# Kernel tuning notes

Measured on AMD Instinct MI355X. Metric: run time of the kernel, lower is better.

## Reference

```python
import jax, jax.numpy as jnp
import numpy as np

B, S, N, D, T = 128, 128, 196, 512, 12


def setup_inputs() -> dict:
    key = jax.random.key(0)
    ks = jax.random.split(key, 20)
    nrm = lambda i, shape, s: jax.random.normal(ks[i], shape, jnp.float32) * s
    w = lambda i, shape: nrm(i, shape, 1.0 / np.sqrt(shape[-1]))
    return {
        "ctx": nrm(0, (B, S, D), 1.0),
        "q": nrm(1, (B, 2 * D), 1.0),
        "k": nrm(2, (B, D, N), 1.0),
        "mem0": nrm(3, (1, D), 0.02),
        "ctrl0": nrm(4, (1, D), 0.02),
        # ControlUnit params
        "Wp": w(5, (T, D, 2 * D)), "bp": jnp.zeros((T, D), jnp.float32),
        "Wcq": w(6, (D, 2 * D)), "bcq": jnp.zeros((D,), jnp.float32),
        "Wca": w(7, (1, D)), "bca": jnp.zeros((1,), jnp.float32),
        # ReadUnit params
        "Wrm": w(8, (D, D)), "brm": jnp.zeros((D,), jnp.float32),
        "Wrc": w(9, (D, 2 * D)), "brc": jnp.zeros((D,), jnp.float32),
        "Wra": w(10, (1, D)), "bra": jnp.zeros((1,), jnp.float32),
        # WriteUnit params
        "Wwc": w(11, (D, 2 * D)), "bwc": jnp.zeros((D,), jnp.float32),
    }


def reference(ctx, q, k, mem0, ctrl0, Wp, bp, Wcq, bcq, Wca, bca,
              Wrm, brm, Wrc, brc, Wra, bra, Wwc, bwc):
    b = q.shape[0]
    c = jnp.broadcast_to(ctrl0, (b, D))
    m = jnp.broadcast_to(mem0, (b, D))
    for t in range(T):
        # --- control unit (alpha_entmax with alpha=1.0 == softmax) ---
        p = q @ Wp[t].T + bp[t]                                # [B, D]
        cc = jnp.concatenate([c, p], axis=1) @ Wcq.T + bcq     # [B, D]
        ctx_p = cc[:, None, :] * ctx                           # [B, S, D]
        aw = jax.nn.softmax(ctx_p @ Wca.T + bca, axis=1)       # [B, S, 1]
        c = (aw * ctx).sum(axis=1)                             # [B, D]
        # --- read unit ---
        mm = (m @ Wrm.T + brm)[:, :, None]                     # [B, D, 1]
        kc = jnp.concatenate([mm * k, k], axis=1)              # [B, 2D, N]
        rc = kc.transpose(0, 2, 1) @ Wrc.T + brc               # [B, N, D]
        logit = ((rc * c[:, None, :]) @ Wra.T + bra)[..., 0]   # [B, N]
        rw = jax.nn.softmax(logit, axis=1)[:, None, :]         # [B, 1, N]
        r = (rw * k).sum(axis=2)                               # [B, D]
        # --- write unit (no self-attention / memory gate) ---
        m = jnp.concatenate([r, m], axis=1) @ Wwc.T + bwc      # [B, D]
    return m
```

## Files before the change

kernel.cpp:

```cpp
#include <hip/hip_runtime.h>
#include <hip/hip_bf16.h>
#include <cstdint>

#define D  512
#define D2 1024
#define BB 128
#define SS 128
#define NN 196
#define TT 12

typedef unsigned short u16;
typedef __attribute__((ext_vector_type(8))) short short8v;
typedef __attribute__((ext_vector_type(4))) float f32x4;

__device__ __forceinline__ float bf2f(u16 h){
  union { unsigned int u; float f; } v; v.u = ((unsigned int)h) << 16; return v.f;
}

__device__ __forceinline__ float LDX(const void* p, size_t i, int isbf){
  if (isbf) return bf2f(((const u16*)p)[i]);
  return ((const float*)p)[i];
}

__device__ __forceinline__ float4 LD4(const void* p, size_t i, int isbf){
  if (isbf){
    ushort4 w = *(const ushort4*)((const u16*)p + i);
    return make_float4(bf2f(w.x), bf2f(w.y), bf2f(w.z), bf2f(w.w));
  }
  return *(const float4*)((const float*)p + i);
}

__device__ __forceinline__ void bfsplit(float x, short &h, short &l){
  unsigned u = __float_as_uint(x);
  unsigned hu = u & 0xFFFF0000u;
  float r = x - __uint_as_float(hu);
  h = (short)(u >> 16);
  l = (short)(__float_as_uint(r) >> 16);
}

__global__ __launch_bounds__(256) void k_detect(const u16* ctx, int* flag){
  __shared__ int cnt;
  if (threadIdx.x == 0) cnt = 0;
  __syncthreads();
  int bad = 0;
  for (int i = threadIdx.x; i < 8192; i += 256){
    int e = (ctx[i] >> 7) & 0xFF;
    if (e == 0xFF || (e != 0 && (e < 90 || e > 160))) bad++;
  }
  atomicAdd(&cnt, bad);
  __syncthreads();
  if (threadIdx.x == 0) *flag = (cnt > 100) ? 0 : 1;
}

__global__ __launch_bounds__(256) void k_prep1(const void* Wcq, const void* Wca,
      const void* Wwc, const void* Wrm, const void* Wrc, const void* Wra,
      const void* bp, const void* bcq, const void* ctrl0, const void* mem0, const void* brm,
      float* W1f, float* Wwcf, float* WrmTf, float* W2f,
      float* P, float* pp2, float* ubase, float* mmb, const int* flag){
  const int isbf = *flag;
  __shared__ float lds[32][33];
  int bk = blockIdx.x, tid = threadIdx.x;
  int tx = tid & 31, ty = tid >> 5;
  if (bk >= 1216){
    int ib = bk - 1216;
    int lane = tid & 63, w = tid >> 6;
    int grp = lane >> 3, k = lane & 7;
    int isU = (ib < 16);
    int o = (isU ? ib : ib - 16)*32 + w*8 + grp;
    const void* vec = isU ? ctrl0 : mem0;
    const void* mat = isU ? Wcq : Wrm;
    int ld = isU ? D2 : D;
    float acc = 0.f;
    #pragma unroll 4
    for (int it = 0; it < 16; it++){
      int d = it*32 + k*4;
      float4 v = LD4(vec, d, isbf);
      float4 m = LD4(mat, (size_t)o*ld + d, isbf);
      acc += v.x*m.x + v.y*m.y + v.z*m.z + v.w*m.w;
    }
    acc += __shfl_xor(acc, 1, 64);
    acc += __shfl_xor(acc, 2, 64);
    acc += __shfl_xor(acc, 4, 64);
    if (k == 0){
      if (isU) ubase[o] = acc * LDX(Wca, o, isbf);
      else     mmb[o]   = acc + LDX(brm, o, isbf);
    }
    return;
  }
  if (bk >= 1152){
    int l = bk - 1152;
    for (int idx = l*256 + tid; idx < 786432; idx += 64*256){
      int j = (idx >> 7) & 511;
      pp2[idx] = LDX(bcq, j, isbf) * LDX(Wca, j, isbf);
    }
    return;
  }
  if (bk >= 1088){
    int l = bk - 1088;
    for (int idx = l*256 + tid; idx < 786432; idx += 64*256)
      P[idx] = LDX(bp, idx >> 7, isbf);
    return;
  }
  if (bk >= 1024){
    int l = bk - 1024;
    if (isbf){
      const u16* w = (const u16*)Wrc; const u16* s = (const u16*)Wra;
      for (int idx = l*256 + tid; idx < 524288; idx += 64*256)
        W2f[idx] = bf2f(w[idx]) * bf2f(s[idx >> 10]);
    } else {
      const float* w = (const float*)Wrc; const float* s = (const float*)Wra;
      for (int idx = l*256 + tid; idx < 524288; idx += 64*256)
        W2f[idx] = w[idx] * s[idx >> 10];
    }
    return;
  }
  const void* in = nullptr; const void* scale = nullptr; float* out = nullptr;
  int ld = 0, R = 0, tR = 0, tC = 0;
  if (bk < 256)      { int l = bk;       in = Wcq; ld = 1024; R = 512; out = W1f;  scale = Wca; tR = l & 15; tC = l >> 4; }
  else if (bk < 768) { int l = bk - 256; in = Wwc; ld = 1024; R = 512; out = Wwcf; tR = l & 15; tC = l >> 4; }
  else               { int l = bk - 768; in = Wrm; ld = 512;  R = 512; out = WrmTf;tR = l & 15; tC = l >> 4; }
  int r0 = tR*32, c0 = tC*32;
  #pragma unroll
  for (int kk = 0; kk < 4; kk++){
    int r = r0 + ty + kk*8;
    float v = LDX(in, (size_t)r*ld + c0 + tx, isbf);
    if (scale) v *= LDX(scale, r, isbf);
    lds[tx][ty + kk*8] = v;
  }
  __syncthreads();
  #pragma unroll
  for (int kk = 0; kk < 4; kk++){
    int oc = ty + kk*8;
    out[(size_t)(c0 + oc)*R + r0 + tx] = lds[oc][tx];
  }
}

__global__ __launch_bounds__(256) void k_pack(const void* q, u16* QF,
                                              const void* kmat, float* kT, const int* flag){
  const int isbf = *flag;
  __shared__ float lds[64][201];
  int bk = blockIdx.x, tid = threadIdx.x;
  if (bk < 128){
    u16* QH = QF;
    u16* QL = QF + 131072;
    for (int idx = bk*256 + tid; idx < 131072; idx += 128*256){
      int b = idx >> 10, x = idx & 1023;
      int o = ((x >> 3) << 10) + (b << 3) + (x & 7);
      if (isbf){
        QH[o] = ((const u16*)q)[idx];
        QL[o] = 0;
      } else {
        short h, l;
        bfsplit(((const float*)q)[idx], h, l);
        QH[o] = (u16)h;
        QL[o] = (u16)l;
      }
    }
    return;
  }
  int l = bk - 128;
  int b = l >> 3, dt = l & 7;
  int d0 = dt*64;
  int r = tid >> 2, q4 = tid & 3;
  const size_t rowbase = ((size_t)b*D + d0 + r)*NN;
  #pragma unroll
  for (int p = 0; p < 13; p++){
// ... 88 lines not shown
    const u16* w = (const u16*)Wcq;
    for (int e = e0k; e < e0k + 256; e += 8){
      float a[8];
      #pragma unroll
      for (int u = 0; u < 8; u++) a[u] = P[(size_t)(t*D + e + u)*BB + b];
      #pragma unroll
      for (int kk = 0; kk < 4; kk++){
        ushort4 w0 = *(const ushort4*)(w + (size_t)(j0+kk)*D2 + D + e);
        ushort4 w1 = *(const ushort4*)(w + (size_t)(j0+kk)*D2 + D + e + 4);
        acc[kk] += a[0]*bf2f(w0.x) + a[1]*bf2f(w0.y) + a[2]*bf2f(w0.z) + a[3]*bf2f(w0.w)
                 + a[4]*bf2f(w1.x) + a[5]*bf2f(w1.y) + a[6]*bf2f(w1.z) + a[7]*bf2f(w1.w);
      }
    }
  } else {
    const float* w = (const float*)Wcq;
    for (int e = e0k; e < e0k + 256; e += 8){
      float a[8];
      #pragma unroll
      for (int u = 0; u < 8; u++) a[u] = P[(size_t)(t*D + e + u)*BB + b];
      #pragma unroll
      for (int kk = 0; kk < 4; kk++){
        float4 w0 = *(const float4*)(w + (size_t)(j0+kk)*D2 + D + e);
        float4 w1 = *(const float4*)(w + (size_t)(j0+kk)*D2 + D + e + 4);
        acc[kk] += a[0]*w0.x + a[1]*w0.y + a[2]*w0.z + a[3]*w0.w
                 + a[4]*w1.x + a[5]*w1.y + a[6]*w1.z + a[7]*w1.w;
      }
    }
  }
  #pragma unroll
  for (int kk = 0; kk < 4; kk++)
    atomicAdd(&pp2[(size_t)(t*D + j0 + kk)*BB + b], acc[kk] * LDX(Wca, j0 + kk, isbf));
}

__global__ __launch_bounds__(256) void k_initB(const float* ubase, const float* mmb,
                                               const void* mem0, const float* pp2,
                                               float* u0, float* mm0, float* act0,
                                               const int* flag){
  const int isbf = *flag;
  for (int idx = blockIdx.x*256 + threadIdx.x; idx < 3*D*BB; idx += 96*256){
    if (idx < D*BB)            u0[idx] = ubase[idx >> 7] + pp2[idx];
    else if (idx < 2*D*BB)   { int x = idx - D*BB;   mm0[x] = mmb[x >> 7]; }
    else                     { int x = idx - 2*D*BB; act0[D*BB + x] = LDX(mem0, x >> 7, isbf); }
  }
}

__global__ __launch_bounds__(512) void k_K1(const void* ctx, const float* u_cur,
                                            float* gbuf, const float* pbuf, const float* kT,
                                            float* r_out, int t, const int* flag){
  __shared__ float sm[1024];
  int bk = blockIdx.x, tid = threadIdx.x;
  const int isbf = *flag;
  if (bk < 512){
    if (t == 0) return;
    float* lg   = sm;
    float* red  = sm + 256;
    float* psum = sm + 512;
    int b = bk & 127, qc = bk >> 7;
    if (tid < 256){
      float s;
      if (tid < NN){
        s = 0.f;
        #pragma unroll
        for (int c = 0; c < 8; c++)
          s += pbuf[((size_t)c*BB + b)*256 + tid];
      } else s = -INFINITY;
      lg[tid] = s; red[tid] = s;
    }
    __syncthreads();
    for (int off = 128; off; off >>= 1){ if (tid < off) red[tid] = fmaxf(red[tid], red[tid+off]); __syncthreads(); }
    float M = red[0];
    __syncthreads();
    if (tid < 256){ float e = (tid < NN) ? __expf(lg[tid] - M) : 0.f; lg[tid] = e; red[tid] = e; }
    __syncthreads();
    for (int off = 128; off; off >>= 1){ if (tid < off) red[tid] += red[tid+off]; __syncthreads(); }
    float inv = 1.f / red[0];
    int ng = tid >> 7, dl = tid & 127;
    const float* kTb = kT + ((size_t)b*NN + ng*49)*D + qc*128 + dl;
    float acc = 0.f;
    for (int j = 0; j < 49; j++)
      acc += lg[ng*49 + j] * kTb[(size_t)j*D];
    psum[ng*128 + dl] = acc;
    __syncthreads();
    if (tid < 128)
      r_out[(size_t)(qc*128 + tid)*BB + b] =
        (psum[tid] + psum[128 + tid] + psum[256 + tid] + psum[384 + tid]) * inv;
    return;
  }
  if (t >= TT) return;
  int l = bk - 512;
  int b = l & 127, sc = l >> 7;
  float* us = sm;
  us[tid] = u_cur[(size_t)tid*BB + b];
  __syncthreads();
  int lane = tid & 63, wv = tid >> 6;
  float ur[8];
  #pragma unroll
  for (int j = 0; j < 8; j++) ur[j] = us[lane*8 + j];
  #pragma unroll
  for (int rr = 0; rr < 4; rr++){
    int s = sc*32 + wv*4 + rr;
    size_t base = ((size_t)(b*SS + s))*D + lane*8;
    float4 c0 = LD4(ctx, base, isbf);
    float4 c1 = LD4(ctx, base + 4, isbf);
    float dot = ur[0]*c0.x + ur[1]*c0.y + ur[2]*c0.z + ur[3]*c0.w
              + ur[4]*c1.x + ur[5]*c1.y + ur[6]*c1.z + ur[7]*c1.w;
    #pragma unroll
    for (int off = 32; off; off >>= 1) dot += __shfl_down(dot, off, 64);
    if (lane == 0) gbuf[b*SS + s] = dot;
  }
}

__global__ __launch_bounds__(512) void k_K2(const void* ctx, const float* gbuf, float* cbuf,
                                            const float* act_prev, float* act_cur,
                                            float* wbuf, float* mmbuf, float* u_nxt,
                                            const float* pp2_next, const void* brm,
                                            const float* Wwcf, int t, const int* flag){
  __shared__ float sm[768];
  int bk = blockIdx.x, tid = threadIdx.x;
  const int isbf = *flag;
  if (bk < 512){
    float* lg   = sm;
    float* red  = sm + 128;
    float* psum = sm + 256;
    int b = bk & 127, qc = bk >> 7;
    if (tid < 128){ float v = gbuf[b*SS + tid]; lg[tid] = v; red[tid] = v; }
    __syncthreads();
    for (int off = 64; off; off >>= 1){ if (tid < off) red[tid] = fmaxf(red[tid], red[tid+off]); __syncthreads(); }
    float M = red[0];
    __syncthreads();
    if (tid < 128){ float e = __expf(lg[tid] - M); lg[tid] = e; red[tid] = e; }
    __syncthreads();
    for (int off = 64; off; off >>= 1){ if (tid < off) red[tid] += red[tid+off]; __syncthreads(); }
    float inv = 1.f / red[0];
    int sg = tid >> 7, dl = tid & 127;
    int d = qc*128 + dl;
    float acc = 0.f;
    for (int j = 0; j < 32; j++){
      int s = sg*32 + j;
      acc += lg[s] * LDX(ctx, ((size_t)(b*SS + s))*D + d, isbf);
    }
    psum[sg*128 + dl] = acc;
    __syncthreads();
    if (tid < 128)
      cbuf[(size_t)(qc*128 + tid)*BB + b] =
        (psum[tid] + psum[128 + tid] + psum[256 + tid] + psum[384 + tid]) * inv;
    return;
  }
  int b = tid & 127;
  int ih = __builtin_amdgcn_readfirstlane(tid >> 7);
  if (bk < 1024){
    if (t == 0) return;
    int l = bk - 512;
    int it = l >> 3, kc = l & 7;
    int ih0 = ih & 1, ih1 = ih >> 1;
    int i0 = it*8 + ih0*4;
    int e0 = kc*128 + ih1*64;
    float acc[4] = {0.f,0.f,0.f,0.f};
    for (int e = e0; e < e0 + 64; e += 8){
      float av[8];
      #pragma unroll
      for (int u = 0; u < 8; u++) av[u] = act_prev[(size_t)(e+u)*BB + b];
      #pragma unroll
      for (int u = 0; u < 8; u++){
        float4 w0 = *(const float4*)(Wwcf + (size_t)(e+u)*D + i0);
        acc[0]+=av[u]*w0.x; acc[1]+=av[u]*w0.y; acc[2]+=av[u]*w0.z; acc[3]+=av[u]*w0.w;
      }
    }
    #pragma unroll
    for (int kk = 0; kk < 4; kk++)
      atomicAdd(&act_cur[(size_t)(D + i0 + kk)*BB + b], acc[kk]);
  } else if (bk < 1088){
    int l = bk - 1024;
    for (int x = l*512 + tid; x < D2*BB; x += 64*512) wbuf[x] = 0.f;
  } else if (bk < 1120){
    if (t == 0) return;
    int l = bk - 1088;
    for (int x = l*512 + tid; x < D*BB; x += 32*512) mmbuf[x] = LDX(brm, x >> 7, isbf);
  } else {
    if (t >= TT-1) return;
    int l = bk - 1120;
    for (int x = l*512 + tid; x < D*BB; x += 32*512) u_nxt[x] = pp2_next[x];
  }
}

__global__ __launch_bounds__(256) void k_KB(const float* cbuf, const float* W2f, float* wbuf,
                                            const float* act_cur, const float* WrmTf,
                                            float* mmbuf, int t){
  int bk = blockIdx.x, tid = threadIdx.x;
  int b = tid & 127;
  int ih = __builtin_amdgcn_readfirstlane(tid >> 7);
  if (bk < 512){
    int et = bk >> 2, kc = bk & 3;
    int e0 = et*8 + ih*4;
    float acc[4] = {0.f, 0.f, 0.f, 0.f};
    int j0 = kc*128;
    for (int j = j0; j < j0 + 128; j += 8){
      float av[8];
      #pragma unroll
      for (int u = 0; u < 8; u++) av[u] = cbuf[(j+u)*BB + b];
      #pragma unroll
      for (int u = 0; u < 8; u++){
        float4 wv = *(const float4*)(W2f + (size_t)(j+u)*D2 + e0);
        acc[0] += av[u]*wv.x; acc[1] += av[u]*wv.y;
        acc[2] += av[u]*wv.z; acc[3] += av[u]*wv.w;
      }
    }
    #pragma unroll
    for (int kk = 0; kk < 4; kk++) atomicAdd(&wbuf[(e0+kk)*BB + b], acc[kk]);
  } else {
    if (t == 0) return;
    int l = bk - 512;
    int it = l >> 2, kc = l & 3;
    int i0 = it*8 + ih*4;
    float acc[4] = {0.f, 0.f, 0.f, 0.f};
    int d0 = kc*128;
    for (int d = d0; d < d0 + 128; d += 8){
      float av[8];
      #pragma unroll
      for (int u = 0; u < 8; u++) av[u] = act_cur[(size_t)(D + d + u)*BB + b];
      #pragma unroll
      for (int u = 0; u < 8; u++){
        float4 wv = *(const float4*)(WrmTf + (size_t)(d+u)*D + i0);
        acc[0] += av[u]*wv.x; acc[1] += av[u]*wv.y;
        acc[2] += av[u]*wv.z; acc[3] += av[u]*wv.w;
      }
    }
    #pragma unroll
    for (int kk = 0; kk < 4; kk++) atomicAdd(&mmbuf[(i0+kk)*BB + b], acc[kk]);
  }
}

__global__ __launch_bounds__(512) void k_KC1(const void* kmat, const float* wbuf,
                                             const float* mmbuf, float* pbuf,
                                             const float* cbuf, const float* W1f, float* u_nxt,
                                             float* act_nxt, const void* bwc,
                                             int t, const int* flag){
  __shared__ float u2[128];
  int bk = blockIdx.x, tid = threadIdx.x;
  const int isbf = *flag;
  if (bk < 512){
    int b = bk & 127, ch2 = bk >> 7;
    int d0 = ch2*128;
    if (tid < 128){
      int d = d0 + tid;
      u2[tid] = wbuf[(size_t)d*BB + b]*mmbuf[(size_t)d*BB + b] + wbuf[(size_t)(D + d)*BB + b];
    }
    __syncthreads();
    int half = tid >> 8;
    int n = tid & 255;
    int dd0 = half*64;
    float part = 0.f;
    if (n < NN){
      float c[8];
      #pragma unroll
      for (int u = 0; u < 8; u++) c[u] = 0.f;
      if (isbf){
        const u16* kb = (const u16*)kmat + (size_t)b*D*NN + (size_t)(d0+dd0)*NN + n;
        for (int dd = 0; dd < 64; dd += 8){
          #pragma unroll
          for (int u = 0; u < 8; u++) c[u] += u2[dd0+dd+u]*bf2f(kb[(size_t)(dd+u)*NN]);
        }
      } else {
        const float* kb = (const float*)kmat + (size_t)b*D*NN + (size_t)(d0+dd0)*NN + n;
        for (int dd = 0; dd < 64; dd += 8){
          #pragma unroll
          for (int u = 0; u < 8; u++) c[u] += u2[dd0+dd+u]*kb[(size_t)(dd+u)*NN];
        }
      }
      part = (((c[0]+c[1]) + (c[2]+c[3])) + ((c[4]+c[5]) + (c[6]+c[7])));
    }
    int chunk = ch2*2 + half;
    pbuf[((size_t)chunk*BB + b)*256 + n] = part;
    return;
  }
  int b = tid & 127;
  int ih = __builtin_amdgcn_readfirstlane(tid >> 7);
  if (bk < 768){
    if (t >= TT-1) return;
    int l = bk - 512;
// ... 73 lines not shown
    }
  }
}

extern "C" void kernel_launch(void* const* d_in, const int* in_sizes, int n_in,
                              void* d_out, int out_size, void* d_ws, size_t ws_size,
                              hipStream_t stream){
  const void* ctx  = d_in[0];
  const void* q    = d_in[1];
  const void* kmat = d_in[2];
  const void* mem0 = d_in[3];
  const void* ctrl0= d_in[4];
  const void* Wp   = d_in[5];
  const void* bp   = d_in[6];
  const void* Wcq  = d_in[7];
  const void* bcq  = d_in[8];
  const void* Wca  = d_in[9];
  const void* Wrm  = d_in[11];
  const void* brm  = d_in[12];
  const void* Wrc  = d_in[13];
  const void* Wra  = d_in[15];
  const void* Wwc  = d_in[17];
  const void* bwc  = d_in[18];

  float* W      = (float*)d_ws;
  float* qT     = W;
  float* P      = W + 131072;
  float* pp2    = W + 917504;
  float* W1f    = W + 1703936;
  float* W2f    = W + 1966080;
  float* Wwcf   = W + 2490368;
  float* WrmTf  = W + 3014656;
  float* cbuf   = W + 3276800;
  float* wbuf   = W + 3342336;
  float* mmbuf  = W + 3473408;
  float* actb   = W + 3538944;
  float* ubuf   = W + 3801088;
  int*   flag   = (int*)(W + 3932160);
  float* ubase  = W + 3932224;
  float* mmb    = W + 3932736;
  float* gbuf   = W + 3933248;
  float* pbuf   = P;
  float* kT     = W + 4194304;

  hipLaunchKernelGGL(k_detect, dim3(1), dim3(256), 0, stream, (const u16*)ctx, flag);
  hipLaunchKernelGGL(k_prep1, dim3(1248), dim3(256), 0, stream,
                     Wcq, Wca, Wwc, Wrm, Wrc, Wra, bp, bcq, ctrl0, mem0, brm,
                     W1f, Wwcf, WrmTf, W2f, P, pp2, ubase, mmb, flag);
  hipLaunchKernelGGL(k_pack, dim3(1152), dim3(256), 0, stream,
                     q, (u16*)qT, kmat, kT, flag);
  hipLaunchKernelGGL(k_Pmfma, dim3(768), dim3(256), 0, stream, Wp, (const u16*)qT, P, flag);
  hipLaunchKernelGGL(k_pp2,  dim3(768), dim3(512), 0, stream, P, Wcq, Wca, pp2, flag);
  hipLaunchKernelGGL(k_initB, dim3(96), dim3(256), 0, stream,
                     ubase, mmb, mem0, pp2, ubuf, mmbuf, actb, flag);

  for (int t = 0; t < TT; t++){
    int cur = t & 1, nxt = 1 - cur;
    float* act_cur  = actb + cur*131072;
    float* act_prev = actb + nxt*131072;
    hipLaunchKernelGGL(k_K1, dim3(1024), dim3(512), 0, stream,
                       ctx, ubuf + cur*65536, gbuf, pbuf, kT,
                       act_prev, t, flag);
    hipLaunchKernelGGL(k_K2, dim3(1152), dim3(512), 0, stream,
                       ctx, gbuf, cbuf, act_prev, act_cur,
                       wbuf, mmbuf, ubuf + nxt*65536,
                       pp2 + ((t+1 < TT) ? (t+1)*65536 : 0), brm, Wwcf, t, flag);
    hipLaunchKernelGGL(k_KB, dim3(768), dim3(256), 0, stream,
                       cbuf, W2f, wbuf, act_cur, WrmTf, mmbuf, t);
    hipLaunchKernelGGL(k_KC1, dim3(800), dim3(512), 0, stream,
                       kmat, wbuf, mmbuf, pbuf,
                       cbuf, W1f, ubuf + nxt*65536,
                       actb + nxt*131072, bwc, t, flag);
  }
  hipLaunchKernelGGL(k_K1, dim3(512), dim3(512), 0, stream,
                     ctx, ubuf, gbuf, pbuf, kT,
                     actb + 131072, TT, flag);
  hipLaunchKernelGGL(k_moutA, dim3(512), dim3(512), 0, stream,
                     actb + 131072, Wwcf, actb);
  hipLaunchKernelGGL(k_outT, dim3(64), dim3(256), 0, stream, actb, d_out, flag);
}
```

Before: 1.017 ms.

## Precompose Wwc·Wrm and merge attention kernels to cut per-step launches

```diff
diff --git a/kernel.cpp b/kernel.cpp
--- a/kernel.cpp
+++ b/kernel.cpp
@@ -55,8 +55,9 @@
 __global__ __launch_bounds__(256) void k_prep1(const void* Wcq, const void* Wca,
       const void* Wwc, const void* Wrm, const void* Wrc, const void* Wra,
       const void* bp, const void* bcq, const void* ctrl0, const void* mem0, const void* brm,
+      const void* bwc,
       float* W1f, float* Wwcf, float* WrmTf, float* W2f,
-      float* P, float* pp2, float* ubase, float* mmb, const int* flag){
+      float* P, float* pp2, float* ubase, float* mmb, float* mmc, const int* flag){
   const int isbf = *flag;
   __shared__ float lds[32][33];
   int bk = blockIdx.x, tid = threadIdx.x;
@@ -65,11 +66,11 @@
     int ib = bk - 1216;
     int lane = tid & 63, w = tid >> 6;
     int grp = lane >> 3, k = lane & 7;
-    int isU = (ib < 16);
-    int o = (isU ? ib : ib - 16)*32 + w*8 + grp;
-    const void* vec = isU ? ctrl0 : mem0;
-    const void* mat = isU ? Wcq : Wrm;
-    int ld = isU ? D2 : D;
+    int kind = ib >> 4;
+    int o = (ib & 15)*32 + w*8 + grp;
+    const void* vec = (kind == 0) ? ctrl0 : ((kind == 1) ? mem0 : bwc);
+    const void* mat = (kind == 0) ? Wcq : Wrm;
+    int ld = (kind == 0) ? D2 : D;
     float acc = 0.f;
     #pragma unroll 4
     for (int it = 0; it < 16; it++){
@@ -82,8 +83,9 @@
     acc += __shfl_xor(acc, 2, 64);
     acc += __shfl_xor(acc, 4, 64);
     if (k == 0){
-      if (isU) ubase[o] = acc * LDX(Wca, o, isbf);
-      else     mmb[o]   = acc + LDX(brm, o, isbf);
+      if (kind == 0)      ubase[o] = acc * LDX(Wca, o, isbf);
+      else if (kind == 1) mmb[o]   = acc + LDX(brm, o, isbf);
+      else                mmc[o]   = acc + LDX(brm, o, isbf);
     }
     return;
   }
@@ -132,6 +134,26 @@
   for (int kk = 0; kk < 4; kk++){
     int oc = ty + kk*8;
     out[(size_t)(c0 + oc)*R + r0 + tx] = lds[oc][tx];
+  }
+}
+
+__global__ __launch_bounds__(256) void k_gf(const float* Wwcf, const float* WrmTf, float* GF){
+  __shared__ float wr[4][512];
+  int o0 = blockIdx.x * 4, tid = threadIdx.x;
+  for (int idx = tid; idx < 4*512; idx += 256)
+    wr[idx >> 9][idx & 511] = Wwcf[(size_t)(o0 + (idx >> 9))*D + (idx & 511)];
+  __syncthreads();
+  float a0[4] = {0.f,0.f,0.f,0.f}, a1[4] = {0.f,0.f,0.f,0.f};
+  for (int j = 0; j < 512; j++){
+    float x = WrmTf[(size_t)j*D + tid];
+    float y = WrmTf[(size_t)j*D + 256 + tid];
+    #pragma unroll
+    for (int r = 0; r < 4; r++){ a0[r] += wr[r][j]*x; a1[r] += wr[r][j]*y; }
+  }
+  #pragma unroll
+  for (int r = 0; r < 4; r++){
+    GF[(size_t)(o0 + r)*D + tid]       = a0[r];
+    GF[(size_t)(o0 + r)*D + 256 + tid] = a1[r];
   }
 }
 
@@ -298,9 +320,10 @@
   }
 }
 
-__global__ __launch_bounds__(512) void k_K1(const void* ctx, const float* u_cur,
-                                            float* gbuf, const float* pbuf, const float* kT,
-                                            float* r_out, int t, const int* flag){
+__global__ __launch_bounds__(512) void k_KA2(const void* ctx, const float* u_cur,
+      const float* pbuf, const float* kT, float* cbuf, float* r_out,
+      float* wbuf, float* mmbuf, float* u_nxt, const float* pp2_next,
+      const float* mmb, const float* mmc, int t, const int* flag){
   __shared__ float sm[1024];
   int bk = blockIdx.x, tid = threadIdx.x;
   const int isbf = *flag;
@@ -340,44 +363,31 @@
         (psum[tid] + psum[128 + tid] + psum[256 + tid] + psum[384 + tid]) * inv;
     return;
   }
-  if (t >= TT) return;
-  int l = bk - 512;
-  int b = l & 127, sc = l >> 7;
-  float* us = sm;
-  us[tid] = u_cur[(size_t)tid*BB + b];
-  __syncthreads();
-  int lane = tid & 63, wv = tid >> 6;
-  float ur[8];
-  #pragma unroll
-  for (int j = 0; j < 8; j++) ur[j] = us[lane*8 + j];
-  #pragma unroll
-  for (int rr = 0; rr < 4; rr++){
-    int s = sc*32 + wv*4 + rr;
-    size_t base = ((size_t)(b*SS + s))*D + lane*8;
-    float4 c0 = LD4(ctx, base, isbf);
-    float4 c1 = LD4(ctx, base + 4, isbf);
-    float dot = ur[0]*c0.x + ur[1]*c0.y + ur[2]*c0.z + ur[3]*c0.w
-              + ur[4]*c1.x + ur[5]*c1.y + ur[6]*c1.z + ur[7]*c1.w;
-    #pragma unroll
-    for (int off = 32; off; off >>= 1) dot += __shfl_down(dot, off, 64);
-    if (lane == 0) gbuf[b*SS + s] = dot;
-  }
-}
-
-__global__ __launch_bounds__(512) void k_K2(const void* ctx, const float* gbuf, float* cbuf,
-                                            const float* act_prev, float* act_cur,
-                                            float* wbuf, float* mmbuf, float* u_nxt,
-                                            const float* pp2_next, const void* brm,
-                                            const float* Wwcf, int t, const int* flag){
-  __shared__ float sm[768];
-  int bk = blockIdx.x, tid = threadIdx.x;
-  const int isbf = *flag;
-  if (bk < 512){
-    float* lg   = sm;
-    float* red  = sm + 128;
-    float* psum = sm + 256;
-    int b = bk & 127, qc = bk >> 7;
-    if (tid < 128){ float v = gbuf[b*SS + tid]; lg[tid] = v; red[tid] = v; }
+  if (bk < 640){
+    if (t >= TT) return;
+    int b = bk - 512;
+    float* us  = sm;
+    float* lg  = sm + 512;
+    float* red = sm + 640;
+    us[tid] = u_cur[(size_t)tid*BB + b];
+    __syncthreads();
+    int lane = tid & 63, wv = tid >> 6;
+    float ur[8];
+    #pragma unroll
+    for (int j = 0; j < 8; j++) ur[j] = us[lane*8 + j];
+    for (int rr = 0; rr < 16; rr++){
+      int s = wv*16 + rr;
+      size_t base = ((size_t)(b*SS + s))*D + lane*8;
+      float4 c0 = LD4(ctx, base, isbf);
+      float4 c1 = LD4(ctx, base + 4, isbf);
+      float dot = ur[0]*c0.x + ur[1]*c0.y + ur[2]*c0.z + ur[3]*c0.w
+                + ur[4]*c1.x + ur[5]*c1.y + ur[6]*c1.z + ur[7]*c1.w;
+      #pragma unroll
+      for (int off = 32; off; off >>= 1) dot += __shfl_down(dot, off, 64);
+      if (lane == 0) lg[s] = dot;
+    }
+    __syncthreads();
+    if (tid < 128) red[tid] = lg[tid];
     __syncthreads();
     for (int off = 64; off; off >>= 1){ if (tid < off) red[tid] = fmaxf(red[tid], red[tid+off]); __syncthreads(); }
     float M = red[0];
@@ -386,66 +396,37 @@
     __syncthreads();
     for (int off = 64; off; off >>= 1){ if (tid < off) red[tid] += red[tid+off]; __syncthreads(); }
     float inv = 1.f / red[0];
-    int sg = tid >> 7, dl = tid & 127;
-    int d = qc*128 + dl;
     float acc = 0.f;
-    for (int j = 0; j < 32; j++){
-      int s = sg*32 + j;
-      acc += lg[s] * LDX(ctx, ((size_t)(b*SS + s))*D + d, isbf);
-    }
-    psum[sg*128 + dl] = acc;
-    __syncthreads();
-    if (tid < 128)
-      cbuf[(size_t)(qc*128 + tid)*BB + b] =
-        (psum[tid] + psum[128 + tid] + psum[256 + tid] + psum[384 + tid]) * inv;
-    return;
-  }
-  int b = tid & 127;
-  int ih = __builtin_amdgcn_readfirstlane(tid >> 7);
-  if (bk < 1024){
-    if (t == 0) return;
-    int l = bk - 512;
-    int it = l >> 3, kc = l & 7;
-    int ih0 = ih & 1, ih1 = ih >> 1;
-    int i0 = it*8 + ih0*4;
-    int e0 = kc*128 + ih1*64;
-    float acc[4] = {0.f,0.f,0.f,0.f};
-    for (int e = e0; e < e0 + 64; e += 8){
-      float av[8];
-      #pragma unroll
-      for (int u = 0; u < 8; u++) av[u] = act_prev[(size_t)(e+u)*BB + b];
-      #pragma unroll
-      for (int u = 0; u < 8; u++){
-        float4 w0 = *(const float4*)(Wwcf + (size_t)(e+u)*D + i0);
-        acc[0]+=av[u]*w0.x; acc[1]+=av[u]*w0.y; acc[2]+=av[u]*w0.z; acc[3]+=av[u]*w0.w;
-      }
-    }
-    #pragma unroll
-    for (int kk = 0; kk < 4; kk++)
-      atomicAdd(&act_cur[(size_t)(D + i0 + kk)*BB + b], acc[kk]);
-  } else if (bk < 1088){
-    int l = bk - 1024;
-    for (int x = l*512 + tid; x < D2*BB; x += 64*512) wbuf[x] = 0.f;
-  } else if (bk < 1120){
-    if (t == 0) return;
-    int l = bk - 1088;
-    for (int x = l*512 + tid; x < D*BB; x += 32*512) mmbuf[x] = LDX(brm, x >> 7, isbf);
+    #pragma unroll 8
+    for (int s = 0; s < SS; s++)
+      acc += lg[s] * LDX(ctx, ((size_t)(b*SS + s))*D + tid, isbf);
+    cbuf[(size_t)tid*BB + b] = acc * inv;
+    return;
+  }
+  if (bk < 656){
+    int l = bk - 640;
+    for (int x = l*512 + tid; x < D2*BB; x += 16*512) wbuf[x] = 0.f;
+  } else if (bk < 664){
+    int l = bk - 656;
+    const float* src = (t == 0) ? mmb : mmc;
+    for (int x = l*512 + tid; x < D*BB; x += 8*512) mmbuf[x] = src[x >> 7];
   } else {
     if (t >= TT-1) return;
-    int l = bk - 1120;
-    for (int x = l*512 + tid; x < D*BB; x += 32*512) u_nxt[x] = pp2_next[x];
-  }
-}
-
-__global__ __launch_bounds__(256) void k_KB(const float* cbuf, const float* W2f, float* wbuf,
-                                            const float* act_cur, const float* WrmTf,
-                                            float* mmbuf, int t){
+    int l = bk - 664;
+    for (int x = l*512 + tid; x < D*BB; x += 8*512) u_nxt[x] = pp2_next[x];
+  }
+}
+
+__global__ __launch_bounds__(512) void k_KB2(const float* cbuf, const float* W2f, float* wbuf,
+                                             const float* act_prev, const float* GF,
+                                             float* mmbuf, const float* Wwcf, float* act_cur,
+                                             int t){
   int bk = blockIdx.x, tid = threadIdx.x;
   int b = tid & 127;
   int ih = __builtin_amdgcn_readfirstlane(tid >> 7);
-  if (bk < 512){
+  if (bk < 256){
     int et = bk >> 2, kc = bk & 3;
-    int e0 = et*8 + ih*4;
+    int e0 = et*16 + ih*4;
     float acc[4] = {0.f, 0.f, 0.f, 0.f};
     int j0 = kc*128;
     for (int j = j0; j < j0 + 128; j += 8){
@@ -461,27 +442,31 @@
     }
     #pragma unroll
     for (int kk = 0; kk < 4; kk++) atomicAdd(&wbuf[(e0+kk)*BB + b], acc[kk]);
-  } else {
-    if (t == 0) return;
-    int l = bk - 512;
-    int it = l >> 2, kc = l & 3;
-    int i0 = it*8 + ih*4;
-    float acc[4] = {0.f, 0.f, 0.f, 0.f};
-    int d0 = kc*128;
-    for (int d = d0; d < d0 + 128; d += 8){
-      float av[8];
-      #pragma unroll
-      for (int u = 0; u < 8; u++) av[u] = act_cur[(size_t)(D + d + u)*BB + b];
-      #pragma unroll
-      for (int u = 0; u < 8; u++){
-        float4 wv = *(const float4*)(WrmTf + (size_t)(d+u)*D + i0);
-        acc[0] += av[u]*wv.x; acc[1] += av[u]*wv.y;
-        acc[2] += av[u]*wv.z; acc[3] += av[u]*wv.w;
-      }
-    }
-    #pragma unroll
-    for (int kk = 0; kk < 4; kk++) atomicAdd(&mmbuf[(i0+kk)*BB + b], acc[kk]);
-  }
+    return;
+  }
+  if (t == 0) return;
+  const float* Mx; float* outp; int obase;
+  int l;
+  if (bk < 768){ l = bk - 256; Mx = GF;   outp = mmbuf;   obase = 0; }
+  else         { l = bk - 768; Mx = Wwcf; outp = act_cur; obase = D; }
+  int it = l >> 3, kc = l & 7;
+  int ih0 = ih & 1, ih1 = ih >> 1;
+  int i0 = it*8 + ih0*4;
+  int e0 = kc*128 + ih1*64;
+  float acc[4] = {0.f,0.f,0.f,0.f};
+  for (int e = e0; e < e0 + 64; e += 8){
+    float av[8];
+    #pragma unroll
+    for (int u = 0; u < 8; u++) av[u] = act_prev[(size_t)(e+u)*BB + b];
+    #pragma unroll
+    for (int u = 0; u < 8; u++){
+      float4 w0 = *(const float4*)(Mx + (size_t)(e+u)*D + i0);
+      acc[0]+=av[u]*w0.x; acc[1]+=av[u]*w0.y; acc[2]+=av[u]*w0.z; acc[3]+=av[u]*w0.w;
+    }
+  }
+  #pragma unroll
+  for (int kk = 0; kk < 4; kk++)
+    atomicAdd(&outp[(size_t)(obase + i0 + kk)*BB + b], acc[kk]);
 }
 
 __global__ __launch_bounds__(512) void k_KC1(const void* kmat, const float* wbuf,
@@ -645,17 +630,19 @@
   int*   flag   = (int*)(W + 3932160);
   float* ubase  = W + 3932224;
   float* mmb    = W + 3932736;
-  float* gbuf   = W + 3933248;
+  float* mmc    = W + 3933248;
   float* pbuf   = P;
   float* kT     = W + 4194304;
+  float* GF     = W + 17039360;
 
   hipLaunchKernelGGL(k_detect, dim3(1), dim3(256), 0, stream, (const u16*)ctx, flag);
-  hipLaunchKernelGGL(k_prep1, dim3(1248), dim3(256), 0, stream,
-                     Wcq, Wca, Wwc, Wrm, Wrc, Wra, bp, bcq, ctrl0, mem0, brm,
-                     W1f, Wwcf, WrmTf, W2f, P, pp2, ubase, mmb, flag);
+  hipLaunchKernelGGL(k_prep1, dim3(1264), dim3(256), 0, stream,
+                     Wcq, Wca, Wwc, Wrm, Wrc, Wra, bp, bcq, ctrl0, mem0, brm, bwc,
+                     W1f, Wwcf, WrmTf, W2f, P, pp2, ubase, mmb, mmc, flag);
   hipLaunchKernelGGL(k_pack, dim3(1152), dim3(256), 0, stream,
                      q, (u16*)qT, kmat, kT, flag);
   hipLaunchKernelGGL(k_Pmfma, dim3(768), dim3(256), 0, stream, Wp, (const u16*)qT, P, flag);
+  hipLaunchKernelGGL(k_gf, dim3(256), dim3(256), 0, stream, Wwcf, WrmTf, GF);
   hipLaunchKernelGGL(k_pp2,  dim3(768), dim3(512), 0, stream, P, Wcq, Wca, pp2, flag);
   hipLaunchKernelGGL(k_initB, dim3(96), dim3(256), 0, stream,
                      ubase, mmb, mem0, pp2, ubuf, mmbuf, actb, flag);
@@ -664,23 +651,20 @@
     int cur = t & 1, nxt = 1 - cur;
     float* act_cur  = actb + cur*131072;
     float* act_prev = actb + nxt*131072;
-    hipLaunchKernelGGL(k_K1, dim3(1024), dim3(512), 0, stream,
-                       ctx, ubuf + cur*65536, gbuf, pbuf, kT,
-                       act_prev, t, flag);
-    hipLaunchKernelGGL(k_K2, dim3(1152), dim3(512), 0, stream,
-                       ctx, gbuf, cbuf, act_prev, act_cur,
+    hipLaunchKernelGGL(k_KA2, dim3(672), dim3(512), 0, stream,
+                       ctx, ubuf + cur*65536, pbuf, kT, cbuf, act_prev,
                        wbuf, mmbuf, ubuf + nxt*65536,
-                       pp2 + ((t+1 < TT) ? (t+1)*65536 : 0), brm, Wwcf, t, flag);
-    hipLaunchKernelGGL(k_KB, dim3(768), dim3(256), 0, stream,
-                       cbuf, W2f, wbuf, act_cur, WrmTf, mmbuf, t);
+                       pp2 + ((t+1 < TT) ? (t+1)*65536 : 0), mmb, mmc, t, flag);
+    hipLaunchKernelGGL(k_KB2, dim3(1280), dim3(512), 0, stream,
+                       cbuf, W2f, wbuf, act_prev, GF, mmbuf, Wwcf, act_cur, t);
     hipLaunchKernelGGL(k_KC1, dim3(800), dim3(512), 0, stream,
                        kmat, wbuf, mmbuf, pbuf,
                        cbuf, W1f, ubuf + nxt*65536,
                        actb + nxt*131072, bwc, t, flag);
   }
-  hipLaunchKernelGGL(k_K1, dim3(512), dim3(512), 0, stream,
-                     ctx, ubuf, gbuf, pbuf, kT,
-                     actb + 131072, TT, flag);
+  hipLaunchKernelGGL(k_KA2, dim3(512), dim3(512), 0, stream,
+                     ctx, ubuf, pbuf, kT, cbuf, actb + 131072,
+                     wbuf, mmbuf, ubuf, pp2, mmb, mmc, TT, flag);
   hipLaunchKernelGGL(k_moutA, dim3(512), dim3(512), 0, stream,
                      actb + 131072, Wwcf, actb);
   hipLaunchKernelGGL(k_outT, dim3(64), dim3(256), 0, stream, actb, d_out, flag);
```

Result: slower. 1.102 ms (+8.4%).

## Precompose Wrm with Wwc to compute next-step mm directly from previous activations

Applied to the files above, without the earlier changes.

```diff
diff --git a/kernel.cpp b/kernel.cpp
--- a/kernel.cpp
+++ b/kernel.cpp
@@ -55,8 +55,9 @@
 __global__ __launch_bounds__(256) void k_prep1(const void* Wcq, const void* Wca,
       const void* Wwc, const void* Wrm, const void* Wrc, const void* Wra,
       const void* bp, const void* bcq, const void* ctrl0, const void* mem0, const void* brm,
+      const void* bwc,
       float* W1f, float* Wwcf, float* WrmTf, float* W2f,
-      float* P, float* pp2, float* ubase, float* mmb, const int* flag){
+      float* P, float* pp2, float* ubase, float* mmb, float* mmc, const int* flag){
   const int isbf = *flag;
   __shared__ float lds[32][33];
   int bk = blockIdx.x, tid = threadIdx.x;
@@ -65,11 +66,11 @@
     int ib = bk - 1216;
     int lane = tid & 63, w = tid >> 6;
     int grp = lane >> 3, k = lane & 7;
-    int isU = (ib < 16);
-    int o = (isU ? ib : ib - 16)*32 + w*8 + grp;
-    const void* vec = isU ? ctrl0 : mem0;
-    const void* mat = isU ? Wcq : Wrm;
-    int ld = isU ? D2 : D;
+    int kind = ib >> 4;
+    int o = (ib & 15)*32 + w*8 + grp;
+    const void* vec = (kind == 0) ? ctrl0 : ((kind == 1) ? mem0 : bwc);
+    const void* mat = (kind == 0) ? Wcq : Wrm;
+    int ld = (kind == 0) ? D2 : D;
     float acc = 0.f;
     #pragma unroll 4
     for (int it = 0; it < 16; it++){
@@ -82,8 +83,9 @@
     acc += __shfl_xor(acc, 2, 64);
     acc += __shfl_xor(acc, 4, 64);
     if (k == 0){
-      if (isU) ubase[o] = acc * LDX(Wca, o, isbf);
-      else     mmb[o]   = acc + LDX(brm, o, isbf);
+      if (kind == 0)      ubase[o] = acc * LDX(Wca, o, isbf);
+      else if (kind == 1) mmb[o]   = acc + LDX(brm, o, isbf);
+      else                mmc[o]   = acc + LDX(brm, o, isbf);
     }
     return;
   }
@@ -132,6 +134,26 @@
   for (int kk = 0; kk < 4; kk++){
     int oc = ty + kk*8;
     out[(size_t)(c0 + oc)*R + r0 + tx] = lds[oc][tx];
+  }
+}
+
+__global__ __launch_bounds__(256) void k_gf(const float* Wwcf, const float* WrmTf, float* GF){
+  __shared__ float wr[4][512];
+  int o0 = blockIdx.x * 4, tid = threadIdx.x;
+  for (int idx = tid; idx < 4*512; idx += 256)
+    wr[idx >> 9][idx & 511] = Wwcf[(size_t)(o0 + (idx >> 9))*D + (idx & 511)];
+  __syncthreads();
+  float a0[4] = {0.f,0.f,0.f,0.f}, a1[4] = {0.f,0.f,0.f,0.f};
+  for (int j = 0; j < 512; j++){
+    float x = WrmTf[(size_t)j*D + tid];
+    float y = WrmTf[(size_t)j*D + 256 + tid];
+    #pragma unroll
+    for (int r = 0; r < 4; r++){ a0[r] += wr[r][j]*x; a1[r] += wr[r][j]*y; }
+  }
+  #pragma unroll
+  for (int r = 0; r < 4; r++){
+    GF[(size_t)(o0 + r)*D + tid]       = a0[r];
+    GF[(size_t)(o0 + r)*D + 256 + tid] = a1[r];
   }
 }
 
@@ -300,7 +322,8 @@
 
 __global__ __launch_bounds__(512) void k_K1(const void* ctx, const float* u_cur,
                                             float* gbuf, const float* pbuf, const float* kT,
-                                            float* r_out, int t, const int* flag){
+                                            float* r_out, float* mmbuf, const float* mmc,
+                                            int t, const int* flag){
   __shared__ float sm[1024];
   int bk = blockIdx.x, tid = threadIdx.x;
   const int isbf = *flag;
@@ -340,34 +363,40 @@
         (psum[tid] + psum[128 + tid] + psum[256 + tid] + psum[384 + tid]) * inv;
     return;
   }
-  if (t >= TT) return;
-  int l = bk - 512;
-  int b = l & 127, sc = l >> 7;
-  float* us = sm;
-  us[tid] = u_cur[(size_t)tid*BB + b];
-  __syncthreads();
-  int lane = tid & 63, wv = tid >> 6;
-  float ur[8];
-  #pragma unroll
-  for (int j = 0; j < 8; j++) ur[j] = us[lane*8 + j];
-  #pragma unroll
-  for (int rr = 0; rr < 4; rr++){
-    int s = sc*32 + wv*4 + rr;
-    size_t base = ((size_t)(b*SS + s))*D + lane*8;
-    float4 c0 = LD4(ctx, base, isbf);
-    float4 c1 = LD4(ctx, base + 4, isbf);
-    float dot = ur[0]*c0.x + ur[1]*c0.y + ur[2]*c0.z + ur[3]*c0.w
-              + ur[4]*c1.x + ur[5]*c1.y + ur[6]*c1.z + ur[7]*c1.w;
-    #pragma unroll
-    for (int off = 32; off; off >>= 1) dot += __shfl_down(dot, off, 64);
-    if (lane == 0) gbuf[b*SS + s] = dot;
-  }
+  if (bk < 1024){
+    if (t >= TT) return;
+    int l = bk - 512;
+    int b = l & 127, sc = l >> 7;
+    float* us = sm;
+    us[tid] = u_cur[(size_t)tid*BB + b];
+    __syncthreads();
+    int lane = tid & 63, wv = tid >> 6;
+    float ur[8];
+    #pragma unroll
+    for (int j = 0; j < 8; j++) ur[j] = us[lane*8 + j];
+    #pragma unroll
+    for (int rr = 0; rr < 4; rr++){
+      int s = sc*32 + wv*4 + rr;
+      size_t base = ((size_t)(b*SS + s))*D + lane*8;
+      float4 c0 = LD4(ctx, base, isbf);
+      float4 c1 = LD4(ctx, base + 4, isbf);
+      float dot = ur[0]*c0.x + ur[1]*c0.y + ur[2]*c0.z + ur[3]*c0.w
+                + ur[4]*c1.x + ur[5]*c1.y + ur[6]*c1.z + ur[7]*c1.w;
+      #pragma unroll
+      for (int off = 32; off; off >>= 1) dot += __shfl_down(dot, off, 64);
+      if (lane == 0) gbuf[b*SS + s] = dot;
+    }
+    return;
+  }
+  if (t == 0 || t >= TT) return;
+  int l = bk - 1024;
+  for (int x = l*512 + tid; x < D*BB; x += 32*512) mmbuf[x] = mmc[x >> 7];
 }
 
 __global__ __launch_bounds__(512) void k_K2(const void* ctx, const float* gbuf, float* cbuf,
                                             const float* act_prev, float* act_cur,
                                             float* wbuf, float* mmbuf, float* u_nxt,
-                                            const float* pp2_next, const void* brm,
+                                            const float* pp2_next, const float* GF,
                                             const float* Wwcf, int t, const int* flag){
   __shared__ float sm[768];
   int bk = blockIdx.x, tid = threadIdx.x;
@@ -402,9 +431,11 @@
   }
   int b = tid & 127;
   int ih = __builtin_amdgcn_readfirstlane(tid >> 7);
-  if (bk < 1024){
+  if (bk < 1536){
     if (t == 0) return;
-    int l = bk - 512;
+    const float* Mx; float* outp; int obase; int l;
+    if (bk < 1024){ l = bk - 512;  Mx = Wwcf; outp = act_cur; obase = D; }
+    else          { l = bk - 1024; Mx = GF;   outp = mmbuf;   obase = 0; }
     int it = l >> 3, kc = l & 7;
     int ih0 = ih & 1, ih1 = ih >> 1;
     int i0 = it*8 + ih0*4;
@@ -416,72 +447,44 @@
       for (int u = 0; u < 8; u++) av[u] = act_prev[(size_t)(e+u)*BB + b];
       #pragma unroll
       for (int u = 0; u < 8; u++){
-        float4 w0 = *(const float4*)(Wwcf + (size_t)(e+u)*D + i0);
+        float4 w0 = *(const float4*)(Mx + (size_t)(e+u)*D + i0);
         acc[0]+=av[u]*w0.x; acc[1]+=av[u]*w0.y; acc[2]+=av[u]*w0.z; acc[3]+=av[u]*w0.w;
       }
     }
     #pragma unroll
     for (int kk = 0; kk < 4; kk++)
-      atomicAdd(&act_cur[(size_t)(D + i0 + kk)*BB + b], acc[kk]);
-  } else if (bk < 1088){
-    int l = bk - 1024;
+      atomicAdd(&outp[(size_t)(obase + i0 + kk)*BB + b], acc[kk]);
+  } else if (bk < 1600){
+    int l = bk - 1536;
     for (int x = l*512 + tid; x < D2*BB; x += 64*512) wbuf[x] = 0.f;
-  } else if (bk < 1120){
-    if (t == 0) return;
-    int l = bk - 1088;
-    for (int x = l*512 + tid; x < D*BB; x += 32*512) mmbuf[x] = LDX(brm, x >> 7, isbf);
   } else {
     if (t >= TT-1) return;
-    int l = bk - 1120;
+    int l = bk - 1600;
     for (int x = l*512 + tid; x < D*BB; x += 32*512) u_nxt[x] = pp2_next[x];
   }
 }
 
-__global__ __launch_bounds__(256) void k_KB(const float* cbuf, const float* W2f, float* wbuf,
-                                            const float* act_cur, const float* WrmTf,
-                                            float* mmbuf, int t){
+__global__ __launch_bounds__(256) void k_KB(const float* cbuf, const float* W2f, float* wbuf){
   int bk = blockIdx.x, tid = threadIdx.x;
   int b = tid & 127;
   int ih = __builtin_amdgcn_readfirstlane(tid >> 7);
-  if (bk < 512){
-    int et = bk >> 2, kc = bk & 3;
-    int e0 = et*8 + ih*4;
-    float acc[4] = {0.f, 0.f, 0.f, 0.f};
-    int j0 = kc*128;
-    for (int j = j0; j < j0 + 128; j += 8){
-      float av[8];
-      #pragma unroll
-      for (int u = 0; u < 8; u++) av[u] = cbuf[(j+u)*BB + b];
-      #pragma unroll
-      for (int u = 0; u < 8; u++){
-        float4 wv = *(const float4*)(W2f + (size_t)(j+u)*D2 + e0);
-        acc[0] += av[u]*wv.x; acc[1] += av[u]*wv.y;
-        acc[2] += av[u]*wv.z; acc[3] += av[u]*wv.w;
-      }
-    }
-    #pragma unroll
-    for (int kk = 0; kk < 4; kk++) atomicAdd(&wbuf[(e0+kk)*BB + b], acc[kk]);
-  } else {
-    if (t == 0) return;
-    int l = bk - 512;
-    int it = l >> 2, kc = l & 3;
-    int i0 = it*8 + ih*4;
-    float acc[4] = {0.f, 0.f, 0.f, 0.f};
-    int d0 = kc*128;
-    for (int d = d0; d < d0 + 128; d += 8){
-      float av[8];
-      #pragma unroll
-      for (int u = 0; u < 8; u++) av[u] = act_cur[(size_t)(D + d + u)*BB + b];
-      #pragma unroll
-      for (int u = 0; u < 8; u++){
-        float4 wv = *(const float4*)(WrmTf + (size_t)(d+u)*D + i0);
-        acc[0] += av[u]*wv.x; acc[1] += av[u]*wv.y;
-        acc[2] += av[u]*wv.z; acc[3] += av[u]*wv.w;
-      }
-    }
-    #pragma unroll
-    for (int kk = 0; kk < 4; kk++) atomicAdd(&mmbuf[(i0+kk)*BB + b], acc[kk]);
-  }
+  int et = bk >> 2, kc = bk & 3;
+  int e0 = et*8 + ih*4;
+  float acc[4] = {0.f, 0.f, 0.f, 0.f};
+  int j0 = kc*128;
+  for (int j = j0; j < j0 + 128; j += 8){
+    float av[8];
+    #pragma unroll
+    for (int u = 0; u < 8; u++) av[u] = cbuf[(j+u)*BB + b];
+    #pragma unroll
+    for (int u = 0; u < 8; u++){
+      float4 wv = *(const float4*)(W2f + (size_t)(j+u)*D2 + e0);
+      acc[0] += av[u]*wv.x; acc[1] += av[u]*wv.y;
+      acc[2] += av[u]*wv.z; acc[3] += av[u]*wv.w;
+    }
+  }
+  #pragma unroll
+  for (int kk = 0; kk < 4; kk++) atomicAdd(&wbuf[(e0+kk)*BB + b], acc[kk]);
 }
 
 __global__ __launch_bounds__(512) void k_KC1(const void* kmat, const float* wbuf,
@@ -645,17 +648,20 @@
   int*   flag   = (int*)(W + 3932160);
   float* ubase  = W + 3932224;
   float* mmb    = W + 3932736;
-  float* gbuf   = W + 3933248;
+  float* mmc    = W + 3933248;
+  float* gbuf   = W + 3933760;
   float* pbuf   = P;
   float* kT     = W + 4194304;
+  float* GF     = W + 17039360;
 
   hipLaunchKernelGGL(k_detect, dim3(1), dim3(256), 0, stream, (const u16*)ctx, flag);
-  hipLaunchKernelGGL(k_prep1, dim3(1248), dim3(256), 0, stream,
-                     Wcq, Wca, Wwc, Wrm, Wrc, Wra, bp, bcq, ctrl0, mem0, brm,
-                     W1f, Wwcf, WrmTf, W2f, P, pp2, ubase, mmb, flag);
+  hipLaunchKernelGGL(k_prep1, dim3(1264), dim3(256), 0, stream,
+                     Wcq, Wca, Wwc, Wrm, Wrc, Wra, bp, bcq, ctrl0, mem0, brm, bwc,
+                     W1f, Wwcf, WrmTf, W2f, P, pp2, ubase, mmb, mmc, flag);
   hipLaunchKernelGGL(k_pack, dim3(1152), dim3(256), 0, stream,
                      q, (u16*)qT, kmat, kT, flag);
   hipLaunchKernelGGL(k_Pmfma, dim3(768), dim3(256), 0, stream, Wp, (const u16*)qT, P, flag);
+  hipLaunchKernelGGL(k_gf, dim3(256), dim3(256), 0, stream, Wwcf, WrmTf, GF);
   hipLaunchKernelGGL(k_pp2,  dim3(768), dim3(512), 0, stream, P, Wcq, Wca, pp2, flag);
   hipLaunchKernelGGL(k_initB, dim3(96), dim3(256), 0, stream,
                      ubase, mmb, mem0, pp2, ubuf, mmbuf, actb, flag);
@@ -664,15 +670,15 @@
     int cur = t & 1, nxt = 1 - cur;
     float* act_cur  = actb + cur*131072;
     float* act_prev = actb + nxt*131072;
-    hipLaunchKernelGGL(k_K1, dim3(1024), dim3(512), 0, stream,
+    hipLaunchKernelGGL(k_K1, dim3(1056), dim3(512), 0, stream,
                        ctx, ubuf + cur*65536, gbuf, pbuf, kT,
-                       act_prev, t, flag);
-    hipLaunchKernelGGL(k_K2, dim3(1152), dim3(512), 0, stream,
+                       act_prev, mmbuf, mmc, t, flag);
+    hipLaunchKernelGGL(k_K2, dim3(1632), dim3(512), 0, stream,
                        ctx, gbuf, cbuf, act_prev, act_cur,
                        wbuf, mmbuf, ubuf + nxt*65536,
-                       pp2 + ((t+1 < TT) ? (t+1)*65536 : 0), brm, Wwcf, t, flag);
-    hipLaunchKernelGGL(k_KB, dim3(768), dim3(256), 0, stream,
-                       cbuf, W2f, wbuf, act_cur, WrmTf, mmbuf, t);
+                       pp2 + ((t+1 < TT) ? (t+1)*65536 : 0), GF, Wwcf, t, flag);
+    hipLaunchKernelGGL(k_KB, dim3(512), dim3(256), 0, stream,
+                       cbuf, W2f, wbuf);
     hipLaunchKernelGGL(k_KC1, dim3(800), dim3(512), 0, stream,
                        kmat, wbuf, mmbuf, pbuf,
                        cbuf, W1f, ubuf + nxt*65536,
@@ -680,7 +686,7 @@
   }
   hipLaunchKernelGGL(k_K1, dim3(512), dim3(512), 0, stream,
                      ctx, ubuf, gbuf, pbuf, kT,
-                     actb + 131072, TT, flag);
+                     actb + 131072, mmbuf, mmc, TT, flag);
   hipLaunchKernelGGL(k_moutA, dim3(512), dim3(512), 0, stream,
                      actb + 131072, Wwcf, actb);
   hipLaunchKernelGGL(k_outT, dim3(64), dim3(256), 0, stream, actb, d_out, flag);
```

Result: slower. 1.138 ms (+11.9%).

## Fuse KB matvecs into KC1 and drop wbuf/mmbuf zero-init and atomics

Applied to the files above, without the earlier changes.

```diff
diff --git a/kernel.cpp b/kernel.cpp
--- a/kernel.cpp
+++ b/kernel.cpp
@@ -286,15 +286,13 @@
     atomicAdd(&pp2[(size_t)(t*D + j0 + kk)*BB + b], acc[kk] * LDX(Wca, j0 + kk, isbf));
 }
 
-__global__ __launch_bounds__(256) void k_initB(const float* ubase, const float* mmb,
-                                               const void* mem0, const float* pp2,
-                                               float* u0, float* mm0, float* act0,
-                                               const int* flag){
-  const int isbf = *flag;
-  for (int idx = blockIdx.x*256 + threadIdx.x; idx < 3*D*BB; idx += 96*256){
-    if (idx < D*BB)            u0[idx] = ubase[idx >> 7] + pp2[idx];
-    else if (idx < 2*D*BB)   { int x = idx - D*BB;   mm0[x] = mmb[x >> 7]; }
-    else                     { int x = idx - 2*D*BB; act0[D*BB + x] = LDX(mem0, x >> 7, isbf); }
+__global__ __launch_bounds__(256) void k_initB(const float* ubase, const void* mem0,
+                                               const float* pp2,
+                                               float* u0, float* act0, const int* flag){
+  const int isbf = *flag;
+  for (int idx = blockIdx.x*256 + threadIdx.x; idx < 2*D*BB; idx += 64*256){
+    if (idx < D*BB) u0[idx] = ubase[idx >> 7] + pp2[idx];
+    else          { int x = idx - D*BB; act0[D*BB + x] = LDX(mem0, x >> 7, isbf); }
   }
 }
 
@@ -366,8 +364,7 @@
 
 __global__ __launch_bounds__(512) void k_K2(const void* ctx, const float* gbuf, float* cbuf,
                                             const float* act_prev, float* act_cur,
-                                            float* wbuf, float* mmbuf, float* u_nxt,
-                                            const float* pp2_next, const void* brm,
+                                            float* u_nxt, const float* pp2_next,
                                             const float* Wwcf, int t, const int* flag){
   __shared__ float sm[768];
   int bk = blockIdx.x, tid = threadIdx.x;
@@ -423,82 +420,69 @@
     #pragma unroll
     for (int kk = 0; kk < 4; kk++)
       atomicAdd(&act_cur[(size_t)(D + i0 + kk)*BB + b], acc[kk]);
-  } else if (bk < 1088){
-    int l = bk - 1024;
-    for (int x = l*512 + tid; x < D2*BB; x += 64*512) wbuf[x] = 0.f;
-  } else if (bk < 1120){
-    if (t == 0) return;
-    int l = bk - 1088;
-    for (int x = l*512 + tid; x < D*BB; x += 32*512) mmbuf[x] = LDX(brm, x >> 7, isbf);
   } else {
     if (t >= TT-1) return;
-    int l = bk - 1120;
+    int l = bk - 1024;
     for (int x = l*512 + tid; x < D*BB; x += 32*512) u_nxt[x] = pp2_next[x];
   }
 }
 
-__global__ __launch_bounds__(256) void k_KB(const float* cbuf, const float* W2f, float* wbuf,
-                                            const float* act_cur, const float* WrmTf,
-                                            float* mmbuf, int t){
-  int bk = blockIdx.x, tid = threadIdx.x;
-  int b = tid & 127;
-  int ih = __builtin_amdgcn_readfirstlane(tid >> 7);
-  if (bk < 512){
-    int et = bk >> 2, kc = bk & 3;
-    int e0 = et*8 + ih*4;
-    float acc[4] = {0.f, 0.f, 0.f, 0.f};
-    int j0 = kc*128;
-    for (int j = j0; j < j0 + 128; j += 8){
-      float av[8];
-      #pragma unroll
-      for (int u = 0; u < 8; u++) av[u] = cbuf[(j+u)*BB + b];
-      #pragma unroll
-      for (int u = 0; u < 8; u++){
-        float4 wv = *(const float4*)(W2f + (size_t)(j+u)*D2 + e0);
-        acc[0] += av[u]*wv.x; acc[1] += av[u]*wv.y;
-        acc[2] += av[u]*wv.z; acc[3] += av[u]*wv.w;
-      }
-    }
-    #pragma unroll
-    for (int kk = 0; kk < 4; kk++) atomicAdd(&wbuf[(e0+kk)*BB + b], acc[kk]);
-  } else {
-    if (t == 0) return;
-    int l = bk - 512;
-    int it = l >> 2, kc = l & 3;
-    int i0 = it*8 + ih*4;
-    float acc[4] = {0.f, 0.f, 0.f, 0.f};
-    int d0 = kc*128;
-    for (int d = d0; d < d0 + 128; d += 8){
-      float av[8];
-      #pragma unroll
-      for (int u = 0; u < 8; u++) av[u] = act_cur[(size_t)(D + d + u)*BB + b];
-      #pragma unroll
-      for (int u = 0; u < 8; u++){
-        float4 wv = *(const float4*)(WrmTf + (size_t)(d+u)*D + i0);
-        acc[0] += av[u]*wv.x; acc[1] += av[u]*wv.y;
-        acc[2] += av[u]*wv.z; acc[3] += av[u]*wv.w;
-      }
-    }
-    #pragma unroll
-    for (int kk = 0; kk < 4; kk++) atomicAdd(&mmbuf[(i0+kk)*BB + b], acc[kk]);
-  }
-}
-
-__global__ __launch_bounds__(512) void k_KC1(const void* kmat, const float* wbuf,
-                                             const float* mmbuf, float* pbuf,
-                                             const float* cbuf, const float* W1f, float* u_nxt,
+__global__ __launch_bounds__(512) void k_KC1(const void* kmat, const float* cbuf,
+                                             const float* act_cur, const float* W2f,
+                                             const float* WrmTf, const void* brm,
+                                             const float* mmb, float* pbuf,
+                                             const float* W1f, float* u_nxt,
                                              float* act_nxt, const void* bwc,
                                              int t, const int* flag){
+  __shared__ float cb[512];
+  __shared__ float mv[512];
+  __shared__ float wv2[256];
+  __shared__ float mmv[128];
   __shared__ float u2[128];
   int bk = blockIdx.x, tid = threadIdx.x;
   const int isbf = *flag;
   if (bk < 512){
     int b = bk & 127, ch2 = bk >> 7;
     int d0 = ch2*128;
-    if (tid < 128){
-      int d = d0 + tid;
-      u2[tid] = wbuf[(size_t)d*BB + b]*mmbuf[(size_t)d*BB + b] + wbuf[(size_t)(D + d)*BB + b];
-    }
+    cb[tid] = cbuf[(size_t)tid*BB + b];
+    if (t > 0) mv[tid] = act_cur[(size_t)(D + tid)*BB + b];
+    __syncthreads();
+    if (tid < 256){
+      int e = (tid < 128) ? (d0 + tid) : (D + d0 + (tid - 128));
+      float c0=0.f,c1=0.f,c2=0.f,c3=0.f,c4=0.f,c5=0.f,c6=0.f,c7=0.f;
+      for (int j = 0; j < 512; j += 8){
+        c0 += cb[j  ]*W2f[(size_t)(j  )*D2 + e];
+        c1 += cb[j+1]*W2f[(size_t)(j+1)*D2 + e];
+        c2 += cb[j+2]*W2f[(size_t)(j+2)*D2 + e];
+        c3 += cb[j+3]*W2f[(size_t)(j+3)*D2 + e];
+        c4 += cb[j+4]*W2f[(size_t)(j+4)*D2 + e];
+        c5 += cb[j+5]*W2f[(size_t)(j+5)*D2 + e];
+        c6 += cb[j+6]*W2f[(size_t)(j+6)*D2 + e];
+        c7 += cb[j+7]*W2f[(size_t)(j+7)*D2 + e];
+      }
+      wv2[tid] = (((c0+c1)+(c2+c3)) + ((c4+c5)+(c6+c7)));
+    } else if (tid < 384){
+      int tm = tid - 256;
+      int d = d0 + tm;
+      if (t == 0){
+        mmv[tm] = mmb[d];
+      } else {
+        float c0=0.f,c1=0.f,c2=0.f,c3=0.f,c4=0.f,c5=0.f,c6=0.f,c7=0.f;
+        for (int j = 0; j < 512; j += 8){
+          c0 += mv[j  ]*WrmTf[(size_t)(j  )*D + d];
+          c1 += mv[j+1]*WrmTf[(size_t)(j+1)*D + d];
+          c2 += mv[j+2]*WrmTf[(size_t)(j+2)*D + d];
+          c3 += mv[j+3]*WrmTf[(size_t)(j+3)*D + d];
+          c4 += mv[j+4]*WrmTf[(size_t)(j+4)*D + d];
+          c5 += mv[j+5]*WrmTf[(size_t)(j+5)*D + d];
+          c6 += mv[j+6]*WrmTf[(size_t)(j+6)*D + d];
+          c7 += mv[j+7]*WrmTf[(size_t)(j+7)*D + d];
+        }
+        mmv[tm] = LDX(brm, d, isbf) + (((c0+c1)+(c2+c3)) + ((c4+c5)+(c6+c7)));
+      }
+    }
+    __syncthreads();
+    if (tid < 128) u2[tid] = wv2[tid]*mmv[tid] + wv2[128 + tid];
     __syncthreads();
     int half = tid >> 8;
     int n = tid & 255;
@@ -638,8 +622,6 @@
   float* Wwcf   = W + 2490368;
   float* WrmTf  = W + 3014656;
   float* cbuf   = W + 3276800;
-  float* wbuf   = W + 3342336;
-  float* mmbuf  = W + 3473408;
   float* actb   = W + 3538944;
   float* ubuf   = W + 3801088;
   int*   flag   = (int*)(W + 3932160);
@@ -657,8 +639,8 @@
                      q, (u16*)qT, kmat, kT, flag);
   hipLaunchKernelGGL(k_Pmfma, dim3(768), dim3(256), 0, stream, Wp, (const u16*)qT, P, flag);
   hipLaunchKernelGGL(k_pp2,  dim3(768), dim3(512), 0, stream, P, Wcq, Wca, pp2, flag);
-  hipLaunchKernelGGL(k_initB, dim3(96), dim3(256), 0, stream,
-                     ubase, mmb, mem0, pp2, ubuf, mmbuf, actb, flag);
+  hipLaunchKernelGGL(k_initB, dim3(64), dim3(256), 0, stream,
+                     ubase, mem0, pp2, ubuf, actb, flag);
 
   for (int t = 0; t < TT; t++){
     int cur = t & 1, nxt = 1 - cur;
@@ -667,15 +649,13 @@
     hipLaunchKernelGGL(k_K1, dim3(1024), dim3(512), 0, stream,
                        ctx, ubuf + cur*65536, gbuf, pbuf, kT,
                        act_prev, t, flag);
-    hipLaunchKernelGGL(k_K2, dim3(1152), dim3(512), 0, stream,
+    hipLaunchKernelGGL(k_K2, dim3(1056), dim3(512), 0, stream,
                        ctx, gbuf, cbuf, act_prev, act_cur,
-                       wbuf, mmbuf, ubuf + nxt*65536,
-                       pp2 + ((t+1 < TT) ? (t+1)*65536 : 0), brm, Wwcf, t, flag);
-    hipLaunchKernelGGL(k_KB, dim3(768), dim3(256), 0, stream,
-                       cbuf, W2f, wbuf, act_cur, WrmTf, mmbuf, t);
+                       ubuf + nxt*65536,
+                       pp2 + ((t+1 < TT) ? (t+1)*65536 : 0), Wwcf, t, flag);
     hipLaunchKernelGGL(k_KC1, dim3(800), dim3(512), 0, stream,
-                       kmat, wbuf, mmbuf, pbuf,
-                       cbuf, W1f, ubuf + nxt*65536,
+                       kmat, cbuf, act_cur, W2f, WrmTf, brm, mmb, pbuf,
+                       W1f, ubuf + nxt*65536,
                        actb + nxt*131072, bwc, t, flag);
   }
   hipLaunchKernelGGL(k_K1, dim3(512), dim3(512), 0, stream,
```

After: 1.010 ms (median of 3 runs). Within noise of the previous version (-0.7%).
